# Performance work log

Hardware: AMD Instinct MI355X
Metric: run time of the kernel (lower is better)

Reference implementation:

```python
import jax, jax.numpy as jnp
import numpy as np
import math

SPARSITY = 0.95


def _linear(x, W, b):
    # torch nn.Linear: y = x @ W.T + b, W is [out, in]
    return jnp.einsum('bsd,od->bso', x, W) + b


def setup_inputs() -> dict:
    key = jax.random.key(0)
    ks = jax.random.split(key, 11)
    B, S, D = 2, 4096, 512
    std = 1.0 / math.sqrt(D)
    inp = {
        'x': jax.random.normal(ks[0], (B, S, D), dtype=jnp.float32),
        'mask_rand': jax.random.uniform(ks[1], (B, S, S), dtype=jnp.float32),
        'Wq': jax.random.normal(ks[2], (D, D), dtype=jnp.float32) * std,
        'bq': jax.random.normal(ks[3], (D,), dtype=jnp.float32) * std,
        'Wk': jax.random.normal(ks[4], (D, D), dtype=jnp.float32) * std,
        'bk': jax.random.normal(ks[5], (D,), dtype=jnp.float32) * std,
        'Wv': jax.random.normal(ks[6], (D, D), dtype=jnp.float32) * std,
        'bv': jax.random.normal(ks[7], (D,), dtype=jnp.float32) * std,
        'Wo': jax.random.normal(ks[8], (D, D), dtype=jnp.float32) * std,
        'bo': jax.random.normal(ks[9], (D,), dtype=jnp.float32) * std,
    }
    return inp


def reference(x, mask_rand, Wq, bq, Wk, bk, Wv, bv, Wo, bo):
    B, S, D = x.shape
    Q = _linear(x, Wq, bq)
    K = _linear(x, Wk, bk)
    V = _linear(x, Wv, bv)
    scores = jnp.einsum('bqd,bkd->bqk', Q, K) / jnp.sqrt(jnp.asarray(D, x.dtype))
    keep = mask_rand > SPARSITY  # random sparsity mask
    sparse_scores = jnp.where(keep, scores, -jnp.inf)
    attn = jax.nn.softmax(sparse_scores, axis=-1)
    attn_out = jnp.einsum('bqk,bkd->bqd', attn, V)
    # faithful to torch: transpose(1,2).contiguous().view(B, S, D)
    attn_out = jnp.swapaxes(attn_out, 1, 2).reshape(B, S, D)
    return _linear(attn_out, Wo, bo)
```

## Files before the change

kernel.cpp:

```cpp
#include <hip/hip_runtime.h>
#include <hip/hip_bf16.h>
#include <math.h>

typedef __bf16 bf16_t;
typedef __attribute__((ext_vector_type(8))) __bf16 bf16x8;
typedef __attribute__((ext_vector_type(4))) float f32x4;

__device__ __forceinline__ void load16_lds(const bf16_t* g, bf16_t* l) {
    __builtin_amdgcn_global_load_lds(
        (const __attribute__((address_space(1))) void*)g,
        (__attribute__((address_space(3))) void*)l, 16, 0, 0);
}

__global__ __launch_bounds__(256) void cvt_to_bf16(
    const float* __restrict__ src, bf16_t* __restrict__ dst, long n)
{
    const long i = ((long)blockIdx.x * 256 + threadIdx.x) * 4;
    if (i >= n) return;
    const float4 v = *(const float4*)(src + i);
    dst[i + 0] = (bf16_t)v.x;
    dst[i + 1] = (bf16_t)v.y;
    dst[i + 2] = (bf16_t)v.z;
    dst[i + 3] = (bf16_t)v.w;
}

template <int MODE, int F32OUT>
__global__ __launch_bounds__(256) void gemm_bt(
    const bf16_t* __restrict__ A, const bf16_t* __restrict__ B,
    const float* __restrict__ bias, void* __restrict__ Cv,
    int M, int N, int K,
    long sA, long sB, long sC, float scale)
{
    const int b = blockIdx.z;
    A += (long)b * sA;
    B += (long)b * sB;

    __shared__ bf16_t As[128 * 32];
    __shared__ bf16_t Bs[128 * 32];

    const int tid  = threadIdx.x;
    const int wave = tid >> 6;
    const int lane = tid & 63;
    const int quad = lane >> 4;
    const int r16  = lane & 15;
    const int wr   = wave >> 1;
    const int wc   = wave & 1;

    const int m0 = blockIdx.y * 128;
    const int n0 = blockIdx.x * 128;

    const int srow = tid >> 2;
    const int scol = (tid & 3) * 8;

    const bf16_t* gA0 = A + (long)(m0 + srow) * K + scol;
    const bf16_t* gA1 = gA0 + (long)64 * K;
    const bf16_t* gB0 = B + (long)(n0 + srow) * K + scol;
    const bf16_t* gB1 = gB0 + (long)64 * K;
    bf16_t* lA = As + tid * 8;
    bf16_t* lB = Bs + tid * 8;

    f32x4 acc[4][4] = {};

    for (int k0 = 0; k0 < K; k0 += 32) {
        load16_lds(gA0 + k0, lA);
        load16_lds(gA1 + k0, lA + 2048);
        load16_lds(gB0 + k0, lB);
        load16_lds(gB1 + k0, lB + 2048);
        __syncthreads();

        bf16x8 af[4], bfr[4];
#pragma unroll
        for (int i = 0; i < 4; i++)
            af[i] = *(const bf16x8*)(As + (wr * 64 + i * 16 + r16) * 32 + quad * 8);
#pragma unroll
        for (int j = 0; j < 4; j++)
            bfr[j] = *(const bf16x8*)(Bs + (wc * 64 + j * 16 + r16) * 32 + quad * 8);

#pragma unroll
        for (int i = 0; i < 4; i++)
#pragma unroll
            for (int j = 0; j < 4; j++)
                acc[i][j] = __builtin_amdgcn_mfma_f32_16x16x32_bf16(af[i], bfr[j], acc[i][j], 0, 0, 0);
        __syncthreads();
    }

#pragma unroll
    for (int i = 0; i < 4; i++) {
#pragma unroll
        for (int j = 0; j < 4; j++) {
            const int gn = n0 + wc * 64 + j * 16 + r16;
            float bval = 0.f;
            if (MODE == 0) bval = bias[gn];
#pragma unroll
            for (int reg = 0; reg < 4; reg++) {
                const int gm = m0 + wr * 64 + i * 16 + quad * 4 + reg;
                float v = acc[i][j][reg];
                if (MODE == 0) v += bval;
                if (MODE == 1) v *= scale;
                const long cidx = (long)b * sC + (long)gm * N + gn;
                if (F32OUT) ((float*)Cv)[cidx] = v;
                else        ((bf16_t*)Cv)[cidx] = (bf16_t)v;
            }
        }
    }
}

__global__ __launch_bounds__(256) void qkv_gemm(
    const bf16_t* __restrict__ X,
    const bf16_t* __restrict__ Wq, const bf16_t* __restrict__ Wk, const bf16_t* __restrict__ Wv,
    const float* __restrict__ bq, const float* __restrict__ bk, const float* __restrict__ bv,
    bf16_t* __restrict__ Q, bf16_t* __restrict__ Kout, bf16_t* __restrict__ V)
{
    constexpr int K = 512, N = 512;
    const int sel = blockIdx.x >> 2;
    const bf16_t* B = (sel == 0) ? Wq : (sel == 1) ? Wk : Wv;
    const float* bias = (sel == 0) ? bq : (sel == 1) ? bk : bv;
    bf16_t* C = (sel == 0) ? Q : (sel == 1) ? Kout : V;

    __shared__ bf16_t As[128 * 32];
    __shared__ bf16_t Bs[128 * 32];

    const int tid  = threadIdx.x;
    const int wave = tid >> 6;
    const int lane = tid & 63;
    const int quad = lane >> 4;
    const int r16  = lane & 15;
    const int wr   = wave >> 1;
    const int wc   = wave & 1;

    const int m0 = blockIdx.y * 128;
    const int n0 = (blockIdx.x & 3) * 128;

    const int srow = tid >> 2;
    const int scol = (tid & 3) * 8;

    const bf16_t* gA0 = X + (long)(m0 + srow) * K + scol;
    const bf16_t* gA1 = gA0 + (long)64 * K;
    const bf16_t* gB0 = B + (long)(n0 + srow) * K + scol;
    const bf16_t* gB1 = gB0 + (long)64 * K;
    bf16_t* lA = As + tid * 8;
    bf16_t* lB = Bs + tid * 8;

    f32x4 acc[4][4] = {};

    for (int k0 = 0; k0 < K; k0 += 32) {
        load16_lds(gA0 + k0, lA);
        load16_lds(gA1 + k0, lA + 2048);
        load16_lds(gB0 + k0, lB);
        load16_lds(gB1 + k0, lB + 2048);
        __syncthreads();

        bf16x8 af[4], bfr[4];
#pragma unroll
        for (int i = 0; i < 4; i++)
            af[i] = *(const bf16x8*)(As + (wr * 64 + i * 16 + r16) * 32 + quad * 8);
#pragma unroll
        for (int j = 0; j < 4; j++)
            bfr[j] = *(const bf16x8*)(Bs + (wc * 64 + j * 16 + r16) * 32 + quad * 8);

#pragma unroll
        for (int i = 0; i < 4; i++)
#pragma unroll
            for (int j = 0; j < 4; j++)
                acc[i][j] = __builtin_amdgcn_mfma_f32_16x16x32_bf16(af[i], bfr[j], acc[i][j], 0, 0, 0);
        __syncthreads();
    }

#pragma unroll
    for (int i = 0; i < 4; i++) {
#pragma unroll
        for (int j = 0; j < 4; j++) {
            const int gn = n0 + wc * 64 + j * 16 + r16;
            const float bval = bias[gn];
#pragma unroll
            for (int reg = 0; reg < 4; reg++) {
                const int gm = m0 + wr * 64 + i * 16 + quad * 4 + reg;
                C[(long)gm * N + gn] = (bf16_t)(acc[i][j][reg] + bval);
            }
        }
    }
}

__global__ __launch_bounds__(256) void transpose_k(
    const bf16_t* __restrict__ in, bf16_t* __restrict__ out, int rows, int cols)
{
    __shared__ bf16_t tile[32][33];
    const int b = blockIdx.z;
    in  += (long)b * rows * cols;
    out += (long)b * rows * cols;
    const int r0 = blockIdx.y * 32;
    const int c0 = blockIdx.x * 32;
    const int tx = threadIdx.x;
    const int ty = threadIdx.y;
#pragma unroll
    for (int i = 0; i < 4; i++)
        tile[ty + 8 * i][tx] = in[(long)(r0 + ty + 8 * i) * cols + c0 + tx];
    __syncthreads();
#pragma unroll
    for (int i = 0; i < 4; i++)
        out[(long)(c0 + ty + 8 * i) * rows + r0 + tx] = tile[tx][ty + 8 * i];
}

__global__ __launch_bounds__(256) void softmax_mask(
    bf16_t* __restrict__ P, const float* __restrict__ mask)
{
    const long row = blockIdx.x;
    bf16_t* p = P + row * 4096;
    const float* mrow = mask + row * 4096;
    const int tid  = threadIdx.x;
    const int wave = tid >> 6;
    const int lane = tid & 63;
    const int base = tid * 16;

    bf16x8 s0 = *(const bf16x8*)(p + base);
    bf16x8 s1 = *(const bf16x8*)(p + base + 8);
    float mk[16];
#pragma unroll
    for (int c = 0; c < 4; c++) {
        const float4 mv = *(const float4*)(mrow + base + c * 4);
        mk[c * 4 + 0] = mv.x; mk[c * 4 + 1] = mv.y;
        mk[c * 4 + 2] = mv.z; mk[c * 4 + 3] = mv.w;
    }

    float v[16];
    float m = -INFINITY;
#pragma unroll
    for (int i = 0; i < 8; i++) {
        v[i]     = (mk[i]     > 0.95f) ? (float)s0[i] : -INFINITY;
        v[i + 8] = (mk[i + 8] > 0.95f) ? (float)s1[i] : -INFINITY;
    }
#pragma unroll
    for (int i = 0; i < 16; i++) m = fmaxf(m, v[i]);
#pragma unroll
    for (int off = 32; off; off >>= 1) m = fmaxf(m, __shfl_xor(m, off, 64));
    __shared__ float redm[4];
    if (lane == 0) redm[wave] = m;
    __syncthreads();
    m = fmaxf(fmaxf(redm[0], redm[1]), fmaxf(redm[2], redm[3]));

    float s = 0.f;
#pragma unroll
    for (int i = 0; i < 16; i++) {
        v[i] = __expf(v[i] - m);
        s += v[i];
    }
#pragma unroll
    for (int off = 32; off; off >>= 1) s += __shfl_xor(s, off, 64);
    __shared__ float reds[4];
    if (lane == 0) reds[wave] = s;
    __syncthreads();
    s = reds[0] + reds[1] + reds[2] + reds[3];

    const float inv = 1.f / s;
    bf16x8 o0, o1;
#pragma unroll
    for (int i = 0; i < 8; i++) {
        o0[i] = (bf16_t)(v[i] * inv);
        o1[i] = (bf16_t)(v[i + 8] * inv);
    }
    *(bf16x8*)(p + base)     = o0;
    *(bf16x8*)(p + base + 8) = o1;
}

extern "C" void kernel_launch(void* const* d_in, const int* in_sizes, int n_in,
                              void* d_out, int out_size, void* d_ws, size_t ws_size,
                              hipStream_t stream)
{
    constexpr int B = 2, S = 4096, D = 512;
    constexpr int BS = B * S;
    constexpr long QKV_ELEMS = (long)BS * D;
    constexpr long W_ELEMS   = (long)D * D;

    const float* x_raw = (const float*)d_in[0];
    const float* mask  = (const float*)d_in[1];
    const float* Wq    = (const float*)d_in[2];
    const float* bq    = (const float*)d_in[3];
    const float* Wk    = (const float*)d_in[4];
    const float* bk    = (const float*)d_in[5];
    const float* Wv    = (const float*)d_in[6];
    const float* bv    = (const float*)d_in[7];
    const float* Wo    = (const float*)d_in[8];
    const float* bo    = (const float*)d_in[9];

    bf16_t* Q   = (bf16_t*)d_ws;
    bf16_t* Kp  = Q + QKV_ELEMS;
    bf16_t* V   = Kp + QKV_ELEMS;
    bf16_t* VT  = V + QKV_ELEMS;
    bf16_t* T   = V;
    bf16_t* SC  = VT + QKV_ELEMS;
    bf16_t* Xc  = SC + (long)BS * S;
    bf16_t* Wqc = Xc + QKV_ELEMS;
    bf16_t* Wkc = Wqc + W_ELEMS;
    bf16_t* Wvc = Wkc + W_ELEMS;
    bf16_t* Woc = Wvc + W_ELEMS;

    const float scale = 0.044194173824159216f;
    dim3 blk(256);

    cvt_to_bf16<<<dim3((int)(QKV_ELEMS / 1024)), blk, 0, stream>>>(x_raw, Xc, QKV_ELEMS);
    cvt_to_bf16<<<dim3((int)(W_ELEMS / 1024)), blk, 0, stream>>>(Wq, Wqc, W_ELEMS);
    cvt_to_bf16<<<dim3((int)(W_ELEMS / 1024)), blk, 0, stream>>>(Wk, Wkc, W_ELEMS);
    cvt_to_bf16<<<dim3((int)(W_ELEMS / 1024)), blk, 0, stream>>>(Wv, Wvc, W_ELEMS);
    cvt_to_bf16<<<dim3((int)(W_ELEMS / 1024)), blk, 0, stream>>>(Wo, Woc, W_ELEMS);

    qkv_gemm<<<dim3(12, 64), blk, 0, stream>>>(Xc, Wqc, Wkc, Wvc, bq, bk, bv, Q, Kp, V);

    transpose_k<<<dim3(D / 32, S / 32, B), dim3(32, 8), 0, stream>>>(V, VT, S, D);

    gemm_bt<1, 0><<<dim3(S / 128, S / 128, B), blk, 0, stream>>>(Q, Kp, nullptr, SC,
        S, S, D, (long)S * D, (long)S * D, (long)S * S, scale);

    softmax_mask<<<dim3(BS), blk, 0, stream>>>(SC, mask);

    gemm_bt<2, 0><<<dim3(S / 128, D / 128, B), blk, 0, stream>>>(VT, SC, nullptr, T,
        D, S, S, (long)D * S, (long)S * S, (long)D * S, 1.f);

    gemm_bt<0, 1><<<dim3(4, 64, 1), blk, 0, stream>>>(T, Woc, bo, d_out,
        BS, D, D, 0, 0, 0, 0.f);
}
```

Baseline: 411.3 us.

## Fuse masked softmax exp into scores GEMM and split-K the PV GEMM

The scores GEMM epilogue now applies the random mask and computes exp(score*scale) directly, writing unnormalized probabilities and atomically accumulating row sums. This removes the separate softmax kernel and its extra pass over the S×S score matrix. Normalization is deferred to the PV stage, which uses a 4-way split-K with partial buffers and a reduce kernel to raise parallelism. The max subtraction is dropped, so exp overflow is possible for large scores, and the row-sum atomics and partial buffers add traffic.

```diff
diff --git a/kernel.cpp b/kernel.cpp
--- a/kernel.cpp
+++ b/kernel.cpp
@@ -5,6 +5,9 @@
 typedef __bf16 bf16_t;
 typedef __attribute__((ext_vector_type(8))) __bf16 bf16x8;
 typedef __attribute__((ext_vector_type(4))) float f32x4;
+
+constexpr int B_ = 2, S_ = 4096, D_ = 512;
+constexpr int BS_ = B_ * S_;
 
 __device__ __forceinline__ void load16_lds(const bf16_t* g, bf16_t* l) {
     __builtin_amdgcn_global_load_lds(
@@ -24,16 +27,17 @@
     dst[i + 3] = (bf16_t)v.w;
 }
 
-template <int MODE, int F32OUT>
-__global__ __launch_bounds__(256) void gemm_bt(
-    const bf16_t* __restrict__ A, const bf16_t* __restrict__ B,
-    const float* __restrict__ bias, void* __restrict__ Cv,
-    int M, int N, int K,
-    long sA, long sB, long sC, float scale)
-{
-    const int b = blockIdx.z;
-    A += (long)b * sA;
-    B += (long)b * sB;
+__global__ __launch_bounds__(256) void qkv_gemm(
+    const bf16_t* __restrict__ X,
+    const bf16_t* __restrict__ Wq, const bf16_t* __restrict__ Wk, const bf16_t* __restrict__ Wv,
+    const float* __restrict__ bq, const float* __restrict__ bk, const float* __restrict__ bv,
+    bf16_t* __restrict__ Q, bf16_t* __restrict__ Kout, bf16_t* __restrict__ V)
+{
+    constexpr int K = 512, N = 512;
+    const int sel = blockIdx.x >> 2;
+    const bf16_t* B = (sel == 0) ? Wq : (sel == 1) ? Wk : Wv;
+    const float* bias = (sel == 0) ? bq : (sel == 1) ? bk : bv;
+    bf16_t* C = (sel == 0) ? Q : (sel == 1) ? Kout : V;
 
     __shared__ bf16_t As[128 * 32];
     __shared__ bf16_t Bs[128 * 32];
@@ -47,12 +51,12 @@
     const int wc   = wave & 1;
 
     const int m0 = blockIdx.y * 128;
-    const int n0 = blockIdx.x * 128;
+    const int n0 = (blockIdx.x & 3) * 128;
 
     const int srow = tid >> 2;
     const int scol = (tid & 3) * 8;
 
-    const bf16_t* gA0 = A + (long)(m0 + srow) * K + scol;
+    const bf16_t* gA0 = X + (long)(m0 + srow) * K + scol;
     const bf16_t* gA1 = gA0 + (long)64 * K;
     const bf16_t* gB0 = B + (long)(n0 + srow) * K + scol;
     const bf16_t* gB1 = gB0 + (long)64 * K;
@@ -89,36 +93,29 @@
 #pragma unroll
         for (int j = 0; j < 4; j++) {
             const int gn = n0 + wc * 64 + j * 16 + r16;
-            float bval = 0.f;
-            if (MODE == 0) bval = bias[gn];
+            const float bval = bias[gn];
 #pragma unroll
             for (int reg = 0; reg < 4; reg++) {
                 const int gm = m0 + wr * 64 + i * 16 + quad * 4 + reg;
-                float v = acc[i][j][reg];
-                if (MODE == 0) v += bval;
-                if (MODE == 1) v *= scale;
-                const long cidx = (long)b * sC + (long)gm * N + gn;
-                if (F32OUT) ((float*)Cv)[cidx] = v;
-                else        ((bf16_t*)Cv)[cidx] = (bf16_t)v;
+                C[(long)gm * N + gn] = (bf16_t)(acc[i][j][reg] + bval);
             }
         }
     }
 }
 
-__global__ __launch_bounds__(256) void qkv_gemm(
-    const bf16_t* __restrict__ X,
-    const bf16_t* __restrict__ Wq, const bf16_t* __restrict__ Wk, const bf16_t* __restrict__ Wv,
-    const float* __restrict__ bq, const float* __restrict__ bk, const float* __restrict__ bv,
-    bf16_t* __restrict__ Q, bf16_t* __restrict__ Kout, bf16_t* __restrict__ V)
-{
-    constexpr int K = 512, N = 512;
-    const int sel = blockIdx.x >> 2;
-    const bf16_t* B = (sel == 0) ? Wq : (sel == 1) ? Wk : Wv;
-    const float* bias = (sel == 0) ? bq : (sel == 1) ? bk : bv;
-    bf16_t* C = (sel == 0) ? Q : (sel == 1) ? Kout : V;
-
-    __shared__ bf16_t As[128 * 32];
-    __shared__ bf16_t Bs[128 * 32];
+__global__ __launch_bounds__(256) void scores_gemm(
+    const bf16_t* __restrict__ Q, const bf16_t* __restrict__ Km,
+    const float* __restrict__ mask, bf16_t* __restrict__ SC,
+    float* __restrict__ rowsum, float scale)
+{
+    constexpr int S = S_, K = D_;
+    const int b = blockIdx.z;
+    const bf16_t* A = Q + (long)b * S * K;
+    const bf16_t* Bm = Km + (long)b * S * K;
+
+    __shared__ char smem[16384];
+    bf16_t* As = (bf16_t*)smem;
+    bf16_t* Bs = (bf16_t*)(smem + 8192);
 
     const int tid  = threadIdx.x;
     const int wave = tid >> 6;
@@ -129,12 +126,236 @@
     const int wc   = wave & 1;
 
     const int m0 = blockIdx.y * 128;
-    const int n0 = (blockIdx.x & 3) * 128;
+    const int n0 = blockIdx.x * 128;
 
     const int srow = tid >> 2;
     const int scol = (tid & 3) * 8;
 
-    const bf16_t* gA0 = X + (long)(m0 + srow) * K + scol;
+    const bf16_t* gA0 = A + (long)(m0 + srow) * K + scol;
+    const bf16_t* gA1 = gA0 + (long)64 * K;
+    const bf16_t* gB0 = Bm + (long)(n0 + srow) * K + scol;
+    const bf16_t* gB1 = gB0 + (long)64 * K;
+    bf16_t* lA = As + tid * 8;
+    bf16_t* lB = Bs + tid * 8;
+
+    f32x4 acc[4][4] = {};
+
+    for (int k0 = 0; k0 < K; k0 += 32) {
+        load16_lds(gA0 + k0, lA);
+        load16_lds(gA1 + k0, lA + 2048);
+        load16_lds(gB0 + k0, lB);
+        load16_lds(gB1 + k0, lB + 2048);
+        __syncthreads();
+
+        bf16x8 af[4], bfr[4];
+#pragma unroll
+        for (int i = 0; i < 4; i++)
+            af[i] = *(const bf16x8*)(As + (wr * 64 + i * 16 + r16) * 32 + quad * 8);
+#pragma unroll
+        for (int j = 0; j < 4; j++)
+            bfr[j] = *(const bf16x8*)(Bs + (wc * 64 + j * 16 + r16) * 32 + quad * 8);
+
+#pragma unroll
+        for (int i = 0; i < 4; i++)
+#pragma unroll
+            for (int j = 0; j < 4; j++)
+                acc[i][j] = __builtin_amdgcn_mfma_f32_16x16x32_bf16(af[i], bfr[j], acc[i][j], 0, 0, 0);
+        __syncthreads();
+    }
+
+    float* wlds = (float*)smem + wave * 1024;
+    const int erow = lane >> 2;
+    const int ecg  = lane & 3;
+    const long mbase = (long)b * S * S;
+
+#pragma unroll
+    for (int i = 0; i < 4; i++) {
+#pragma unroll
+        for (int j = 0; j < 4; j++)
+#pragma unroll
+            for (int reg = 0; reg < 4; reg++)
+                wlds[(quad * 4 + reg) * 64 + j * 16 + r16] = acc[i][j][reg];
+        __syncthreads();
+
+        float v[16];
+#pragma unroll
+        for (int c = 0; c < 4; c++) {
+            const float4 t = *(const float4*)(wlds + erow * 64 + ecg * 16 + c * 4);
+            v[c * 4 + 0] = t.x; v[c * 4 + 1] = t.y;
+            v[c * 4 + 2] = t.z; v[c * 4 + 3] = t.w;
+        }
+
+        const int gm = m0 + wr * 64 + i * 16 + erow;
+        const int gn = n0 + wc * 64 + ecg * 16;
+        const float* mp = mask + mbase + (long)gm * S + gn;
+
+        float e[16];
+        float rsum = 0.f;
+#pragma unroll
+        for (int c = 0; c < 4; c++) {
+            const float4 mk = *(const float4*)(mp + c * 4);
+            e[c * 4 + 0] = (mk.x > 0.95f) ? __expf(v[c * 4 + 0] * scale) : 0.f;
+            e[c * 4 + 1] = (mk.y > 0.95f) ? __expf(v[c * 4 + 1] * scale) : 0.f;
+            e[c * 4 + 2] = (mk.z > 0.95f) ? __expf(v[c * 4 + 2] * scale) : 0.f;
+            e[c * 4 + 3] = (mk.w > 0.95f) ? __expf(v[c * 4 + 3] * scale) : 0.f;
+        }
+        bf16x8 o0, o1;
+#pragma unroll
+        for (int t = 0; t < 8; t++) {
+            rsum += e[t] + e[t + 8];
+            o0[t] = (bf16_t)e[t];
+            o1[t] = (bf16_t)e[t + 8];
+        }
+        bf16_t* cp = SC + mbase + (long)gm * S + gn;
+        *(bf16x8*)cp       = o0;
+        *(bf16x8*)(cp + 8) = o1;
+
+        rsum += __shfl_xor(rsum, 1, 64);
+        rsum += __shfl_xor(rsum, 2, 64);
+        if (ecg == 0) atomicAdd(&rowsum[b * S + gm], rsum);
+        __syncthreads();
+    }
+}
+
+template <int PMODE, int KS>
+__global__ __launch_bounds__(256) void pv_gemm(
+    const bf16_t* __restrict__ VT, const bf16_t* __restrict__ SC,
+    const float* __restrict__ rowsum, void* __restrict__ outp)
+{
+    constexpr int S = S_, D = D_;
+    constexpr int KC = S / KS;
+    const int z  = blockIdx.z;
+    const int b  = z / KS;
+    const int ks = z % KS;
+
+    const bf16_t* A  = VT + (long)b * D * S;
+    const bf16_t* Bm = SC + (long)b * S * S;
+
+    __shared__ bf16_t As[128 * 32];
+    __shared__ bf16_t Bs[128 * 32];
+
+    const int tid  = threadIdx.x;
+    const int wave = tid >> 6;
+    const int lane = tid & 63;
+    const int quad = lane >> 4;
+    const int r16  = lane & 15;
+    const int wr   = wave >> 1;
+    const int wc   = wave & 1;
+
+    const int m0 = blockIdx.y * 128;
+    const int n0 = blockIdx.x * 128;
+
+    const int srow = tid >> 2;
+    const int scol = (tid & 3) * 8;
+
+    const bf16_t* gA0 = A + (long)(m0 + srow) * S + scol;
+    const bf16_t* gA1 = gA0 + (long)64 * S;
+    const bf16_t* gB0 = Bm + (long)(n0 + srow) * S + scol;
+    const bf16_t* gB1 = gB0 + (long)64 * S;
+    bf16_t* lA = As + tid * 8;
+    bf16_t* lB = Bs + tid * 8;
+
+    f32x4 acc[4][4] = {};
+
+    const int kbeg = ks * KC;
+    const int kend = kbeg + KC;
+    for (int k0 = kbeg; k0 < kend; k0 += 32) {
+        load16_lds(gA0 + k0, lA);
+        load16_lds(gA1 + k0, lA + 2048);
+        load16_lds(gB0 + k0, lB);
+        load16_lds(gB1 + k0, lB + 2048);
+        __syncthreads();
+
+        bf16x8 af[4], bfr[4];
+#pragma unroll
+        for (int i = 0; i < 4; i++)
+            af[i] = *(const bf16x8*)(As + (wr * 64 + i * 16 + r16) * 32 + quad * 8);
+#pragma unroll
+        for (int j = 0; j < 4; j++)
+            bfr[j] = *(const bf16x8*)(Bs + (wc * 64 + j * 16 + r16) * 32 + quad * 8);
+
+#pragma unroll
+        for (int i = 0; i < 4; i++)
+#pragma unroll
+            for (int j = 0; j < 4; j++)
+                acc[i][j] = __builtin_amdgcn_mfma_f32_16x16x32_bf16(af[i], bfr[j], acc[i][j], 0, 0, 0);
+        __syncthreads();
+    }
+
+    const long obase = (PMODE == 2) ? (long)b * D * S
+                                    : ((long)ks * B_ + b) * (long)D * S;
+#pragma unroll
+    for (int i = 0; i < 4; i++) {
+#pragma unroll
+        for (int j = 0; j < 4; j++) {
+            const int gn = n0 + wc * 64 + j * 16 + r16;
+            float inv = 1.f;
+            if (PMODE == 2) inv = 1.f / rowsum[b * S + gn];
+#pragma unroll
+            for (int reg = 0; reg < 4; reg++) {
+                const int gm = m0 + wr * 64 + i * 16 + quad * 4 + reg;
+                const long cidx = obase + (long)gm * S + gn;
+                const float v = acc[i][j][reg];
+                if (PMODE == 0) ((float*)outp)[cidx]  = v;
+                if (PMODE == 1) ((bf16_t*)outp)[cidx] = (bf16_t)v;
+                if (PMODE == 2) ((bf16_t*)outp)[cidx] = (bf16_t)(v * inv);
+            }
+        }
+    }
+}
+
+template <typename PT, int KS>
+__global__ __launch_bounds__(256) void reduce_norm(
+    const PT* __restrict__ part, const float* __restrict__ rowsum,
+    bf16_t* __restrict__ T)
+{
+    constexpr long TOT = (long)B_ * D_ * S_;
+    constexpr long STR = TOT;
+    const long i = ((long)blockIdx.x * 256 + threadIdx.x) * 4;
+    if (i >= TOT) return;
+
+    float s[4] = {0.f, 0.f, 0.f, 0.f};
+#pragma unroll
+    for (int ks = 0; ks < KS; ks++) {
+        const PT* p = part + ks * STR + i;
+#pragma unroll
+        for (int t = 0; t < 4; t++) s[t] += (float)p[t];
+    }
+    const int b = (int)(i / ((long)D_ * S_));
+    const int q = (int)(i & (S_ - 1));
+    const float4 rs = *(const float4*)(rowsum + b * S_ + q);
+    bf16_t o[4];
+    o[0] = (bf16_t)(s[0] / rs.x);
+    o[1] = (bf16_t)(s[1] / rs.y);
+    o[2] = (bf16_t)(s[2] / rs.z);
+    o[3] = (bf16_t)(s[3] / rs.w);
+    *(uint2*)(T + i) = *(uint2*)o;
+}
+
+__global__ __launch_bounds__(256) void out_gemm(
+    const bf16_t* __restrict__ A, const bf16_t* __restrict__ B,
+    const float* __restrict__ bias, float* __restrict__ C)
+{
+    constexpr int N = 512, K = 512;
+
+    __shared__ bf16_t As[128 * 32];
+    __shared__ bf16_t Bs[128 * 32];
+
+    const int tid  = threadIdx.x;
+    const int wave = tid >> 6;
+    const int lane = tid & 63;
+    const int quad = lane >> 4;
+    const int r16  = lane & 15;
+    const int wr   = wave >> 1;
+    const int wc   = wave & 1;
+
+    const int m0 = blockIdx.y * 128;
+    const int n0 = blockIdx.x * 128;
+
+    const int srow = tid >> 2;
+    const int scol = (tid & 3) * 8;
+
+    const bf16_t* gA0 = A + (long)(m0 + srow) * K + scol;
     const bf16_t* gA1 = gA0 + (long)64 * K;
     const bf16_t* gB0 = B + (long)(n0 + srow) * K + scol;
     const bf16_t* gB1 = gB0 + (long)64 * K;
@@ -175,7 +396,7 @@
 #pragma unroll
             for (int reg = 0; reg < 4; reg++) {
                 const int gm = m0 + wr * 64 + i * 16 + quad * 4 + reg;
-                C[(long)gm * N + gn] = (bf16_t)(acc[i][j][reg] + bval);
+                C[(long)gm * N + gn] = acc[i][j][reg] + bval;
             }
         }
     }
@@ -201,75 +422,15 @@
         out[(long)(c0 + ty + 8 * i) * rows + r0 + tx] = tile[tx][ty + 8 * i];
 }
 
-__global__ __launch_bounds__(256) void softmax_mask(
-    bf16_t* __restrict__ P, const float* __restrict__ mask)
-{
-    const long row = blockIdx.x;
-    bf16_t* p = P + row * 4096;
-    const float* mrow = mask + row * 4096;
-    const int tid  = threadIdx.x;
-    const int wave = tid >> 6;
-    const int lane = tid & 63;
-    const int base = tid * 16;
-
-    bf16x8 s0 = *(const bf16x8*)(p + base);
-    bf16x8 s1 = *(const bf16x8*)(p + base + 8);
-    float mk[16];
-#pragma unroll
-    for (int c = 0; c < 4; c++) {
-        const float4 mv = *(const float4*)(mrow + base + c * 4);
-        mk[c * 4 + 0] = mv.x; mk[c * 4 + 1] = mv.y;
-        mk[c * 4 + 2] = mv.z; mk[c * 4 + 3] = mv.w;
-    }
-
-    float v[16];
-    float m = -INFINITY;
-#pragma unroll
-    for (int i = 0; i < 8; i++) {
-        v[i]     = (mk[i]     > 0.95f) ? (float)s0[i] : -INFINITY;
-        v[i + 8] = (mk[i + 8] > 0.95f) ? (float)s1[i] : -INFINITY;
-    }
-#pragma unroll
-    for (int i = 0; i < 16; i++) m = fmaxf(m, v[i]);
-#pragma unroll
-    for (int off = 32; off; off >>= 1) m = fmaxf(m, __shfl_xor(m, off, 64));
-    __shared__ float redm[4];
-    if (lane == 0) redm[wave] = m;
-    __syncthreads();
-    m = fmaxf(fmaxf(redm[0], redm[1]), fmaxf(redm[2], redm[3]));
-
-    float s = 0.f;
-#pragma unroll
-    for (int i = 0; i < 16; i++) {
-        v[i] = __expf(v[i] - m);
-        s += v[i];
-    }
-#pragma unroll
-    for (int off = 32; off; off >>= 1) s += __shfl_xor(s, off, 64);
-    __shared__ float reds[4];
-    if (lane == 0) reds[wave] = s;
-    __syncthreads();
-    s = reds[0] + reds[1] + reds[2] + reds[3];
-
-    const float inv = 1.f / s;
-    bf16x8 o0, o1;
-#pragma unroll
-    for (int i = 0; i < 8; i++) {
-        o0[i] = (bf16_t)(v[i] * inv);
-        o1[i] = (bf16_t)(v[i + 8] * inv);
-    }
-    *(bf16x8*)(p + base)     = o0;
-    *(bf16x8*)(p + base + 8) = o1;
-}
-
 extern "C" void kernel_launch(void* const* d_in, const int* in_sizes, int n_in,
                               void* d_out, int out_size, void* d_ws, size_t ws_size,
                               hipStream_t stream)
 {
-    constexpr int B = 2, S = 4096, D = 512;
-    constexpr int BS = B * S;
+    constexpr int B = B_, S = S_, D = D_;
+    constexpr int BS = BS_;
     constexpr long QKV_ELEMS = (long)BS * D;
     constexpr long W_ELEMS   = (long)D * D;
+    constexpr long SC_ELEMS  = (long)BS * S;
 
     const float* x_raw = (const float*)d_in[0];
     const float* mask  = (const float*)d_in[1];
@@ -282,17 +443,24 @@
     const float* Wo    = (const float*)d_in[8];
     const float* bo    = (const float*)d_in[9];
 
-    bf16_t* Q   = (bf16_t*)d_ws;
-    bf16_t* Kp  = Q + QKV_ELEMS;
-    bf16_t* V   = Kp + QKV_ELEMS;
-    bf16_t* VT  = V + QKV_ELEMS;
+    char* ws = (char*)d_ws;
+    bf16_t* SC  = (bf16_t*)ws;                       ws += SC_ELEMS * 2;
+    bf16_t* VT  = (bf16_t*)ws;                       ws += QKV_ELEMS * 2;
+    bf16_t* Q   = (bf16_t*)ws;                       ws += QKV_ELEMS * 2;
+    bf16_t* Kp  = (bf16_t*)ws;                       ws += QKV_ELEMS * 2;
+    bf16_t* V   = (bf16_t*)ws;                       ws += QKV_ELEMS * 2;
     bf16_t* T   = V;
-    bf16_t* SC  = VT + QKV_ELEMS;
-    bf16_t* Xc  = SC + (long)BS * S;
-    bf16_t* Wqc = Xc + QKV_ELEMS;
-    bf16_t* Wkc = Wqc + W_ELEMS;
-    bf16_t* Wvc = Wkc + W_ELEMS;
-    bf16_t* Woc = Wvc + W_ELEMS;
+    bf16_t* Xc  = (bf16_t*)ws;                       ws += QKV_ELEMS * 2;
+    bf16_t* Wqc = (bf16_t*)ws;                       ws += W_ELEMS * 2;
+    bf16_t* Wkc = (bf16_t*)ws;                       ws += W_ELEMS * 2;
+    bf16_t* Wvc = (bf16_t*)ws;                       ws += W_ELEMS * 2;
+    bf16_t* Woc = (bf16_t*)ws;                       ws += W_ELEMS * 2;
+    float*  rowsum = (float*)ws;                     ws += (long)BS * 4;
+    void*   part = (void*)ws;
+    const size_t used_base = (size_t)(ws - (char*)d_ws);
+    constexpr long PART_ELEMS = 4L * B_ * D_ * S_;
+    const int tier = (ws_size >= used_base + PART_ELEMS * 4) ? 0
+                   : (ws_size >= used_base + PART_ELEMS * 2) ? 1 : 2;
 
     const float scale = 0.044194173824159216f;
     dim3 blk(256);
@@ -307,14 +475,20 @@
 
     transpose_k<<<dim3(D / 32, S / 32, B), dim3(32, 8), 0, stream>>>(V, VT, S, D);
 
-    gemm_bt<1, 0><<<dim3(S / 128, S / 128, B), blk, 0, stream>>>(Q, Kp, nullptr, SC,
-        S, S, D, (long)S * D, (long)S * D, (long)S * S, scale);
-
-    softmax_mask<<<dim3(BS), blk, 0, stream>>>(SC, mask);
-
-    gemm_bt<2, 0><<<dim3(S / 128, D / 128, B), blk, 0, stream>>>(VT, SC, nullptr, T,
-        D, S, S, (long)D * S, (long)S * S, (long)D * S, 1.f);
-
-    gemm_bt<0, 1><<<dim3(4, 64, 1), blk, 0, stream>>>(T, Woc, bo, d_out,
-        BS, D, D, 0, 0, 0, 0.f);
-}
+    hipMemsetAsync(rowsum, 0, (long)BS * 4, stream);
+    scores_gemm<<<dim3(S / 128, S / 128, B), blk, 0, stream>>>(Q, Kp, mask, SC, rowsum, scale);
+
+    if (tier == 0) {
+        pv_gemm<0, 4><<<dim3(S / 128, D / 128, B * 4), blk, 0, stream>>>(VT, SC, rowsum, part);
+        reduce_norm<float, 4><<<dim3((int)(QKV_ELEMS / 1024)), blk, 0, stream>>>(
+            (const float*)part, rowsum, T);
+    } else if (tier == 1) {
+        pv_gemm<1, 4><<<dim3(S / 128, D / 128, B * 4), blk, 0, stream>>>(VT, SC, rowsum, part);
+        reduce_norm<bf16_t, 4><<<dim3((int)(QKV_ELEMS / 1024)), blk, 0, stream>>>(
+            (const bf16_t*)part, rowsum, T);
+    } else {
+        pv_gemm<2, 1><<<dim3(S / 128, D / 128, B), blk, 0, stream>>>(VT, SC, rowsum, T);
+    }
+
+    out_gemm<<<dim3(4, 64), blk, 0, stream>>>(T, Woc, bo, (float*)d_out);
+}
```

New measurement: 395.0 us. -4.0%, faster.
